# Optimization experiments

Measured on AMD Instinct MI355X. Metric: run time of the kernel, lower is better.

The kernel has to match this reference:

```python
import jax, jax.numpy as jnp
import numpy as np

N, F, DE = 768, 64, 32
H0, H1, H2, OUT = 64, 64, 128, 1  # hidden_dim=[64,64,128], output_dim=1


def _mlp(x, Wa, ba, Wb, bb):
    # two Dense layers with relu, as in the repo's MLP
    h = jax.nn.relu(x @ Wa + ba)
    return jax.nn.relu(h @ Wb + bb)


def _edge_conv_e(A, x, e, Wa, ba, Wb, bb):
    # EdgeConvE: per-edge message MLP([x_i, x_j - x_i, e_ij]) aggregated
    # over neighbors j weighted by the (binary) adjacency.
    n = x.shape[0]
    xi = jnp.broadcast_to(x[:, None, :], (n, n, x.shape[1]))  # [N,N,F]
    xj = jnp.broadcast_to(x[None, :, :], (n, n, x.shape[1]))  # [N,N,F]
    feat = jnp.concatenate([xi, xj - xi, e], axis=-1)         # [N,N,2F+De]
    m = _mlp(feat, Wa, ba, Wb, bb)                            # [N,N,H]
    return jnp.einsum('ij,ijh->ih', A, m)                     # scatter-sum over j


def setup_inputs() -> dict:
    key = jax.random.key(0)
    ks = jax.random.split(key, 16)
    adj = (jax.random.uniform(ks[0], (N, N)) < 0.05).astype(jnp.float32)
    x = jax.random.normal(ks[1], (N, F), dtype=jnp.float32)
    e = jax.random.normal(ks[2], (N, N, DE), dtype=jnp.float32)
    s = 0.05
    d_in1 = 2 * F + DE          # 160
    d_in2 = 2 * H0 + DE         # 160
    return {
        'ajacency': adj,
        'node_features': x,
        'edge_attributes': e,
        'W1a': jax.random.normal(ks[3], (d_in1, H0)) * s, 'b1a': jnp.zeros((H0,)),
        'W1b': jax.random.normal(ks[4], (H0, H0)) * s,    'b1b': jnp.zeros((H0,)),
        'W2a': jax.random.normal(ks[5], (d_in2, H1)) * s, 'b2a': jnp.zeros((H1,)),
        'W2b': jax.random.normal(ks[6], (H1, H0)) * s,    'b2b': jnp.zeros((H0,)),
        'W3': jax.random.normal(ks[7], (H0, H2)) * s,     'b3': jnp.zeros((H2,)),
        'W4': jax.random.normal(ks[8], (H2, OUT)) * s,    'b4': jnp.zeros((OUT,)),
    }


def reference(ajacency, node_features, edge_attributes,
              W1a, b1a, W1b, b1b, W2a, b2a, W2b, b2b, W3, b3, W4, b4):
    x = _edge_conv_e(ajacency, node_features, edge_attributes, W1a, b1a, W1b, b1b)
    x = _edge_conv_e(ajacency, x, edge_attributes, W2a, b2a, W2b, b2b)
    x = jax.nn.relu(x @ W3 + b3)
    return jax.nn.sigmoid(x @ W4 + b4)  # [N, OUT]
```

## Files before the change

### kernel.cpp

```cpp
#include <hip/hip_runtime.h>
#include <math.h>


#define NN 768
#define FF 64
#define DE 32
#define HH 64
#define EPB 32
#define CGRID 1024
#define ECAP (NN * 128)
#define SH1S 72

using bf16x8 = __attribute__((ext_vector_type(8))) short;
using f32x4  = __attribute__((ext_vector_type(4))) float;

__device__ __forceinline__ short f2b(float f) {
  unsigned u = __float_as_uint(f);
  return (short)((u + 0x7fffu + ((u >> 16) & 1u)) >> 16);
}

__global__ __launch_bounds__(256) void scan_uv_kernel(
    const float* __restrict__ A, const float* __restrict__ x,
    const float* __restrict__ W, const float* __restrict__ bias,
    const float* __restrict__ Wb1, const float* __restrict__ Wb2,
    int* __restrict__ gcnt, int* __restrict__ edges,
    float* __restrict__ U, float* __restrict__ V,
    float* __restrict__ x1, float* __restrict__ x2,
    short* __restrict__ Wbp1, short* __restrict__ Wbp2)
{
  const int i = blockIdx.x;
  const int tid = threadIdx.x;
  __shared__ int s_cnt, s_base;
  __shared__ int s_j[NN];
  __shared__ float sx[64];
  __shared__ float su[4][64], sv[4][64];

  if (tid == 0) s_cnt = 0;
  __syncthreads();
  if (tid < 64) sx[tid] = x[i * 64 + tid];
  for (int j = tid; j < NN; j += 256) {
    if (A[i * NN + j] != 0.0f) {
      int p = atomicAdd(&s_cnt, 1);
      s_j[p] = j;
    }
  }
  if (tid < 64) { x1[i * 64 + tid] = 0.0f; x2[i * 64 + tid] = 0.0f; }

  if (i < 2) {
    const float* src = (i == 0) ? Wb1 : Wb2;
    short* dst = (i == 0) ? Wbp1 : Wbp2;
    for (int L = tid; L < 4096; L += 256) {
      const int j = L & 7, n = (L >> 3) & 15, quad = (L >> 7) & 3;
      const int kb = (L >> 9) & 1, ct = L >> 10;
      dst[L] = f2b(src[(kb * 32 + quad * 8 + j) * 64 + ct * 16 + n]);
    }
  }
  __syncthreads();

  {
    const int c = tid & 63, qr = tid >> 6;
    float u = 0.0f, v = 0.0f;
#pragma unroll
    for (int t = 0; t < 16; ++t) {
      const int d = qr * 16 + t;
      const float xv = sx[d];
      const float wxi = W[d * 64 + c];
      const float wxj = W[(64 + d) * 64 + c];
      u = fmaf(xv, wxi - wxj, u);
      v = fmaf(xv, wxj, v);
    }
    su[qr][c] = u; sv[qr][c] = v;
  }
  if (tid == 0) s_base = atomicAdd(gcnt, s_cnt);
  __syncthreads();

  if (tid < 64) {
    U[i * 64 + tid] = su[0][tid] + su[1][tid] + su[2][tid] + su[3][tid] + bias[tid];
    V[i * 64 + tid] = sv[0][tid] + sv[1][tid] + sv[2][tid] + sv[3][tid];
  }
  const int c = s_cnt, b = s_base;
  for (int t = tid; t < c; t += 256) edges[b + t] = (i << 10) | s_j[t];
}

__global__ __launch_bounds__(256, 4) void uv_kernel(
    const float* __restrict__ x, const float* __restrict__ W,
    const float* __restrict__ bias, float* __restrict__ U, float* __restrict__ V)
{
  const int tid = threadIdx.x;
  const int rr = tid >> 6, c = tid & 63;
  const int r = blockIdx.x * 4 + rr;
  __shared__ float sx[4][64];
  sx[rr][c] = x[r * 64 + c];
  __syncthreads();
  float u = bias[c], v = 0.0f;
#pragma unroll
  for (int d = 0; d < 64; ++d) {
    float xv = sx[rr][d];
    float wxi = W[d * 64 + c];
    float wxj = W[(64 + d) * 64 + c];
    u = fmaf(xv, wxi - wxj, u);
    v = fmaf(xv, wxj, v);
  }
  U[r * 64 + c] = u;
  V[r * 64 + c] = v;
}

__device__ __forceinline__ void phaseB_mfma(
    const short* __restrict__ sh1b, const int* __restrict__ si,
    const short* __restrict__ Wbp, const float* __restrict__ bb,
    float* __restrict__ xout, int lane, int wv, int nedge)
{
  const int q = lane >> 4, n = lane & 15;
  const int rt = wv >> 1;
  const int ctbase = (wv & 1) * 2;

  bf16x8 bf00 = *(const bf16x8*)(Wbp + ((((ctbase + 0) * 2 + 0) * 4 + q) * 16 + n) * 8);
  bf16x8 bf01 = *(const bf16x8*)(Wbp + ((((ctbase + 0) * 2 + 1) * 4 + q) * 16 + n) * 8);
  bf16x8 bf10 = *(const bf16x8*)(Wbp + ((((ctbase + 1) * 2 + 0) * 4 + q) * 16 + n) * 8);
  bf16x8 bf11 = *(const bf16x8*)(Wbp + ((((ctbase + 1) * 2 + 1) * 4 + q) * 16 + n) * 8);
  const float bias0 = bb[(ctbase + 0) * 16 + n];
  const float bias1 = bb[(ctbase + 1) * 16 + n];

  const short* sa = sh1b + (rt * 16 + n) * SH1S + q * 8;
  bf16x8 a0 = *(const bf16x8*)(sa);
  bf16x8 a1 = *(const bf16x8*)(sa + 32);

  f32x4 acc0 = {0.f, 0.f, 0.f, 0.f}, acc1 = {0.f, 0.f, 0.f, 0.f};
  acc0 = __builtin_amdgcn_mfma_f32_16x16x32_bf16(a0, bf00, acc0, 0, 0, 0);
  acc0 = __builtin_amdgcn_mfma_f32_16x16x32_bf16(a1, bf01, acc0, 0, 0, 0);
  acc1 = __builtin_amdgcn_mfma_f32_16x16x32_bf16(a0, bf10, acc1, 0, 0, 0);
  acc1 = __builtin_amdgcn_mfma_f32_16x16x32_bf16(a1, bf11, acc1, 0, 0, 0);

#pragma unroll
  for (int c2 = 0; c2 < 2; ++c2) {
    const f32x4 d = c2 ? acc1 : acc0;
    const float bias = c2 ? bias1 : bias0;
    const int ch = (ctbase + c2) * 16 + n;
    float sum = 0.0f;
    int cur = -1;
#pragma unroll
    for (int reg = 0; reg < 4; ++reg) {
      const int t = rt * 16 + q * 4 + reg;
      if (t < nedge) {
        const int it = si[t];
        const float v = fmaxf(d[reg] + bias, 0.0f);
        if (it != cur) {
          if (cur >= 0) atomicAdd(&xout[(cur << 6) + ch], sum);
          sum = 0.0f;
          cur = it;
        }
        sum += v;
      }
    }
    if (cur >= 0) atomicAdd(&xout[(cur << 6) + ch], sum);
  }
}

__global__ void conv1_kernel(
    const int* __restrict__ gcnt, const int* __restrict__ edges,
    const float* __restrict__ U, const float* __restrict__ V,
    const float* __restrict__ e, const float* __restrict__ We1,
    const float* __restrict__ We2, const short* __restrict__ Wbp,
    const float* __restrict__ bb, float* __restrict__ xout,
    float* __restrict__ ew2)
{
  const int tid = threadIdx.x, lane = tid & 63, wv = tid >> 6;
  const int M = gcnt[0];
  const int base = blockIdx.x * EPB;
  if (base >= M) return;
  const int nedge = min(EPB, M - base);

  __shared__ __align__(16) short sh1b[EPB * SH1S];
  __shared__ int si[EPB];

  float w1e[DE], w2e[DE];
#pragma unroll
  for (int d = 0; d < DE; ++d) { w1e[d] = We1[d * HH + lane]; w2e[d] = We2[d * HH + lane]; }

  const int a0 = wv * 8;
#pragma unroll
  for (int t = 0; t < 8; ++t) {
    int m = base + a0 + t;
    const bool valid = m < M;
    m = valid ? m : M - 1;
    const int p = edges[m];
    const int i = p >> 10, j = p & 1023;
    float h = U[(i << 6) + lane] + V[(j << 6) + lane];
    float g = 0.0f;
    const float4* ep = (const float4*)(e + ((size_t)i * NN + j) * DE);
#pragma unroll
    for (int u = 0; u < 8; ++u) {
      float4 f = ep[u];
      h = fmaf(f.x, w1e[4 * u + 0], h);
      h = fmaf(f.y, w1e[4 * u + 1], h);
      h = fmaf(f.z, w1e[4 * u + 2], h);
      h = fmaf(f.w, w1e[4 * u + 3], h);
      g = fmaf(f.x, w2e[4 * u + 0], g);
      g = fmaf(f.y, w2e[4 * u + 1], g);
      g = fmaf(f.z, w2e[4 * u + 2], g);
      g = fmaf(f.w, w2e[4 * u + 3], g);
    }
    sh1b[(a0 + t) * SH1S + lane] = f2b(fmaxf(h, 0.0f));
    if (valid) ew2[(size_t)m * HH + lane] = g;
    if (lane == 0) si[a0 + t] = i;
  }
  __syncthreads();

  phaseB_mfma(sh1b, si, Wbp, bb, xout, lane, wv, nedge);
}

__global__ void conv2_kernel(
    const int* __restrict__ gcnt, const int* __restrict__ edges,
    const float* __restrict__ U, const float* __restrict__ V,
    const float* __restrict__ ew2, const short* __restrict__ Wbp,
    const float* __restrict__ bb, float* __restrict__ xout)
{
  const int tid = threadIdx.x, lane = tid & 63, wv = tid >> 6;
  const int M = gcnt[0];
  const int base = blockIdx.x * EPB;
  if (base >= M) return;
  const int nedge = min(EPB, M - base);

  __shared__ __align__(16) short sh1b[EPB * SH1S];
  __shared__ int si[EPB];

  const int a0 = wv * 8;
#pragma unroll
  for (int t = 0; t < 8; ++t) {
    int m = base + a0 + t;
    m = m < M ? m : M - 1;
    const int p = edges[m];
    const int i = p >> 10, j = p & 1023;
    const float h = U[(i << 6) + lane] + V[(j << 6) + lane]
                  + ew2[(size_t)m * HH + lane];
    sh1b[(a0 + t) * SH1S + lane] = f2b(fmaxf(h, 0.0f));
    if (lane == 0) si[a0 + t] = i;
  }
  __syncthreads();

  phaseB_mfma(sh1b, si, Wbp, bb, xout, lane, wv, nedge);
}

__global__ __launch_bounds__(128) void final_kernel(
    const float* __restrict__ x2, const float* __restrict__ W3,
    const float* __restrict__ b3, const float* __restrict__ W4,
    const float* __restrict__ b4, float* __restrict__ out)
{
  const int i = blockIdx.x;
  const int t = threadIdx.x;
  const int lane = t & 63;
  const int wv = t >> 6;
  __shared__ float sx[64];
  __shared__ float s_red[2];
  if (t < 64) sx[t] = x2[i * 64 + t];
  __syncthreads();
  float p = b3[t];
#pragma unroll
  for (int c = 0; c < 64; ++c) p = fmaf(sx[c], W3[c * 128 + t], p);
  p = fmaxf(p, 0.0f);
  float v = p * W4[t];
  v += __shfl_down(v, 32);
  v += __shfl_down(v, 16);
  v += __shfl_down(v, 8);
  v += __shfl_down(v, 4);
  v += __shfl_down(v, 2);
  v += __shfl_down(v, 1);
  if (lane == 0) s_red[wv] = v;
  __syncthreads();
  if (t == 0) {
    float z = s_red[0] + s_red[1] + b4[0];
    out[i] = 1.0f / (1.0f + expf(-z));
  }
}

extern "C" void kernel_launch(void* const* d_in, const int* in_sizes, int n_in,
                              void* d_out, int out_size, void* d_ws, size_t ws_size,
                              hipStream_t stream) {
  const float* A   = (const float*)d_in[0];
  const float* x   = (const float*)d_in[1];
  const float* e   = (const float*)d_in[2];
  const float* W1a = (const float*)d_in[3];
  const float* b1a = (const float*)d_in[4];
  const float* W1b = (const float*)d_in[5];
  const float* b1b = (const float*)d_in[6];
  const float* W2a = (const float*)d_in[7];
  const float* b2a = (const float*)d_in[8];
  const float* W2b = (const float*)d_in[9];
  const float* b2b = (const float*)d_in[10];
  const float* W3  = (const float*)d_in[11];
  const float* b3  = (const float*)d_in[12];
  const float* W4  = (const float*)d_in[13];
  const float* b4  = (const float*)d_in[14];
  float* out = (float*)d_out;

  int*   gcnt  = (int*)d_ws;
  float* x1    = (float*)d_ws + 16;
  float* x2    = x1 + NN * HH;
  float* U1    = x2 + NN * HH;
  float* V1    = U1 + NN * HH;
  float* U2    = V1 + NN * HH;
  float* V2    = U2 + NN * HH;
  int*   edges = (int*)(V2 + NN * HH);
  float* ew2   = (float*)(edges + ECAP);
  short* Wbp1  = (short*)(ew2 + (size_t)CGRID * EPB * HH);
  short* Wbp2  = Wbp1 + 4096;

  hipMemsetAsync(gcnt, 0, 16 * sizeof(int), stream);

  scan_uv_kernel<<<NN, 256, 0, stream>>>(A, x, W1a, b1a, W1b, W2b,
                                         gcnt, edges, U1, V1, x1, x2, Wbp1, Wbp2);
  conv1_kernel<<<CGRID, 256, 0, stream>>>(gcnt, edges, U1, V1, e,
                                          W1a + 128 * HH, W2a + 128 * HH,
                                          Wbp1, b1b, x1, ew2);
  uv_kernel<<<NN / 4, 256, 0, stream>>>(x1, W2a, b2a, U2, V2);
  conv2_kernel<<<CGRID, 256, 0, stream>>>(gcnt, edges, U2, V2, ew2,
                                          Wbp2, b2b, x2);
  final_kernel<<<NN, 128, 0, stream>>>(x2, W3, b3, W4, b4, out);
}
```

Measured before the change: 179.1 us.

## Fuse all five stages into one cooperative persistent kernel with grid syncs

```diff
diff --git a/kernel.cpp b/kernel.cpp
--- a/kernel.cpp
+++ b/kernel.cpp
@@ -1,5 +1,8 @@
 #include <hip/hip_runtime.h>
+#include <hip/hip_cooperative_groups.h>
 #include <math.h>
+
+namespace cg = cooperative_groups;
 
 
 #define NN 768
@@ -7,6 +10,7 @@
 #define DE 32
 #define HH 64
 #define EPB 32
+#define GRID 256
 #define CGRID 1024
 #define ECAP (NN * 128)
 #define SH1S 72
@@ -19,96 +23,10 @@
   return (short)((u + 0x7fffu + ((u >> 16) & 1u)) >> 16);
 }
 
-__global__ __launch_bounds__(256) void scan_uv_kernel(
-    const float* __restrict__ A, const float* __restrict__ x,
-    const float* __restrict__ W, const float* __restrict__ bias,
-    const float* __restrict__ Wb1, const float* __restrict__ Wb2,
-    int* __restrict__ gcnt, int* __restrict__ edges,
-    float* __restrict__ U, float* __restrict__ V,
-    float* __restrict__ x1, float* __restrict__ x2,
-    short* __restrict__ Wbp1, short* __restrict__ Wbp2)
-{
-  const int i = blockIdx.x;
-  const int tid = threadIdx.x;
-  __shared__ int s_cnt, s_base;
-  __shared__ int s_j[NN];
-  __shared__ float sx[64];
-  __shared__ float su[4][64], sv[4][64];
-
-  if (tid == 0) s_cnt = 0;
-  __syncthreads();
-  if (tid < 64) sx[tid] = x[i * 64 + tid];
-  for (int j = tid; j < NN; j += 256) {
-    if (A[i * NN + j] != 0.0f) {
-      int p = atomicAdd(&s_cnt, 1);
-      s_j[p] = j;
-    }
-  }
-  if (tid < 64) { x1[i * 64 + tid] = 0.0f; x2[i * 64 + tid] = 0.0f; }
-
-  if (i < 2) {
-    const float* src = (i == 0) ? Wb1 : Wb2;
-    short* dst = (i == 0) ? Wbp1 : Wbp2;
-    for (int L = tid; L < 4096; L += 256) {
-      const int j = L & 7, n = (L >> 3) & 15, quad = (L >> 7) & 3;
-      const int kb = (L >> 9) & 1, ct = L >> 10;
-      dst[L] = f2b(src[(kb * 32 + quad * 8 + j) * 64 + ct * 16 + n]);
-    }
-  }
-  __syncthreads();
-
-  {
-    const int c = tid & 63, qr = tid >> 6;
-    float u = 0.0f, v = 0.0f;
-#pragma unroll
-    for (int t = 0; t < 16; ++t) {
-      const int d = qr * 16 + t;
-      const float xv = sx[d];
-      const float wxi = W[d * 64 + c];
-      const float wxj = W[(64 + d) * 64 + c];
-      u = fmaf(xv, wxi - wxj, u);
-      v = fmaf(xv, wxj, v);
-    }
-    su[qr][c] = u; sv[qr][c] = v;
-  }
-  if (tid == 0) s_base = atomicAdd(gcnt, s_cnt);
-  __syncthreads();
-
-  if (tid < 64) {
-    U[i * 64 + tid] = su[0][tid] + su[1][tid] + su[2][tid] + su[3][tid] + bias[tid];
-    V[i * 64 + tid] = sv[0][tid] + sv[1][tid] + sv[2][tid] + sv[3][tid];
-  }
-  const int c = s_cnt, b = s_base;
-  for (int t = tid; t < c; t += 256) edges[b + t] = (i << 10) | s_j[t];
-}
-
-__global__ __launch_bounds__(256, 4) void uv_kernel(
-    const float* __restrict__ x, const float* __restrict__ W,
-    const float* __restrict__ bias, float* __restrict__ U, float* __restrict__ V)
-{
-  const int tid = threadIdx.x;
-  const int rr = tid >> 6, c = tid & 63;
-  const int r = blockIdx.x * 4 + rr;
-  __shared__ float sx[4][64];
-  sx[rr][c] = x[r * 64 + c];
-  __syncthreads();
-  float u = bias[c], v = 0.0f;
-#pragma unroll
-  for (int d = 0; d < 64; ++d) {
-    float xv = sx[rr][d];
-    float wxi = W[d * 64 + c];
-    float wxj = W[(64 + d) * 64 + c];
-    u = fmaf(xv, wxi - wxj, u);
-    v = fmaf(xv, wxj, v);
-  }
-  U[r * 64 + c] = u;
-  V[r * 64 + c] = v;
-}
-
 __device__ __forceinline__ void phaseB_mfma(
-    const short* __restrict__ sh1b, const int* __restrict__ si,
-    const short* __restrict__ Wbp, const float* __restrict__ bb,
-    float* __restrict__ xout, int lane, int wv, int nedge)
+    const short* sh1b, const int* si, const short* __restrict__ Wbp,
+    const float* __restrict__ bb, float* __restrict__ xout,
+    int lane, int wv, int nedge)
 {
   const int q = lane >> 4, n = lane & 15;
   const int rt = wv >> 1;
@@ -156,6 +74,282 @@
   }
 }
 
+__global__ __launch_bounds__(256, 2) void mega_kernel(
+    const float* __restrict__ A, const float* __restrict__ x,
+    const float* __restrict__ e,
+    const float* __restrict__ W1a, const float* __restrict__ b1a,
+    const float* __restrict__ W1b, const float* __restrict__ b1b,
+    const float* __restrict__ W2a, const float* __restrict__ b2a,
+    const float* __restrict__ W2b, const float* __restrict__ b2b,
+    const float* __restrict__ W3, const float* __restrict__ b3,
+    const float* __restrict__ W4, const float* __restrict__ b4,
+    float* __restrict__ out,
+    int* gcnt, int* edges, float* x1, float* x2,
+    float* U1, float* V1, float* U2, float* V2,
+    float* ew2, short* Wbp1, short* Wbp2)
+{
+  cg::grid_group grid = cg::this_grid();
+  const int tid = threadIdx.x, lane = tid & 63, wv = tid >> 6;
+  const int bid = blockIdx.x;
+
+  __shared__ int s_cnt, s_base;
+  __shared__ int s_j[NN];
+  __shared__ float sxr[64];
+  __shared__ float su[4][64], sv[4][64];
+  __shared__ __align__(16) short sh1b[EPB * SH1S];
+  __shared__ int si[EPB];
+  __shared__ float sred[4];
+
+  for (int i = bid; i < NN; i += GRID) {
+    __syncthreads();
+    if (tid == 0) s_cnt = 0;
+    __syncthreads();
+    if (tid < 64) sxr[tid] = x[i * 64 + tid];
+    for (int j = tid; j < NN; j += 256) {
+      if (A[i * NN + j] != 0.0f) {
+        int p = atomicAdd(&s_cnt, 1);
+        s_j[p] = j;
+      }
+    }
+    if (tid < 64) { x1[i * 64 + tid] = 0.0f; x2[i * 64 + tid] = 0.0f; }
+    __syncthreads();
+    {
+      const int c = tid & 63, qr = tid >> 6;
+      float u = 0.0f, v = 0.0f;
+#pragma unroll
+      for (int t = 0; t < 16; ++t) {
+        const int d = qr * 16 + t;
+        const float xv = sxr[d];
+        const float wxi = W1a[d * 64 + c];
+        const float wxj = W1a[(64 + d) * 64 + c];
+        u = fmaf(xv, wxi - wxj, u);
+        v = fmaf(xv, wxj, v);
+      }
+      su[qr][c] = u; sv[qr][c] = v;
+    }
+    if (tid == 0) s_base = atomicAdd(gcnt, s_cnt);
+    __syncthreads();
+    if (tid < 64) {
+      U1[i * 64 + tid] = su[0][tid] + su[1][tid] + su[2][tid] + su[3][tid] + b1a[tid];
+      V1[i * 64 + tid] = sv[0][tid] + sv[1][tid] + sv[2][tid] + sv[3][tid];
+    }
+    const int c = s_cnt, b = s_base;
+    for (int t = tid; t < c; t += 256) edges[b + t] = (i << 10) | s_j[t];
+  }
+  if (bid < 2) {
+    const float* src = (bid == 0) ? W1b : W2b;
+    short* dst = (bid == 0) ? Wbp1 : Wbp2;
+    for (int L = tid; L < 4096; L += 256) {
+      const int j = L & 7, n = (L >> 3) & 15, quad = (L >> 7) & 3;
+      const int kb = (L >> 9) & 1, ct = L >> 10;
+      dst[L] = f2b(src[(kb * 32 + quad * 8 + j) * 64 + ct * 16 + n]);
+    }
+  }
+  __threadfence();
+  grid.sync();
+  const int M = gcnt[0];
+
+  {
+    float w1e[DE], w2e[DE];
+#pragma unroll
+    for (int d = 0; d < DE; ++d) {
+      w1e[d] = W1a[(128 + d) * HH + lane];
+      w2e[d] = W2a[(128 + d) * HH + lane];
+    }
+    const int a0 = wv * 8;
+    for (int base = bid * EPB; base < M; base += GRID * EPB) {
+      const int nedge = min(EPB, M - base);
+#pragma unroll
+      for (int t = 0; t < 8; ++t) {
+        int m = base + a0 + t;
+        const bool valid = m < M;
+        m = valid ? m : M - 1;
+        const int p = edges[m];
+        const int i = p >> 10, j = p & 1023;
+        float h = U1[(i << 6) + lane] + V1[(j << 6) + lane];
+        float g = 0.0f;
+        const float4* ep = (const float4*)(e + ((size_t)i * NN + j) * DE);
+#pragma unroll
+        for (int u = 0; u < 8; ++u) {
+          float4 f = ep[u];
+          h = fmaf(f.x, w1e[4 * u + 0], h);
+          h = fmaf(f.y, w1e[4 * u + 1], h);
+          h = fmaf(f.z, w1e[4 * u + 2], h);
+          h = fmaf(f.w, w1e[4 * u + 3], h);
+          g = fmaf(f.x, w2e[4 * u + 0], g);
+          g = fmaf(f.y, w2e[4 * u + 1], g);
+          g = fmaf(f.z, w2e[4 * u + 2], g);
+          g = fmaf(f.w, w2e[4 * u + 3], g);
+        }
+        sh1b[(a0 + t) * SH1S + lane] = f2b(fmaxf(h, 0.0f));
+        if (valid) ew2[(size_t)m * HH + lane] = g;
+        if (lane == 0) si[a0 + t] = i;
+      }
+      __syncthreads();
+      phaseB_mfma(sh1b, si, Wbp1, b1b, x1, lane, wv, nedge);
+      __syncthreads();
+    }
+  }
+  __threadfence();
+  grid.sync();
+
+  for (int r4 = bid; r4 < NN / 4; r4 += GRID) {
+    const int rr = tid >> 6, c = tid & 63;
+    const int r = r4 * 4 + rr;
+    __syncthreads();
+    su[rr][c] = x1[r * 64 + c];
+    __syncthreads();
+    float u = b2a[c], v = 0.0f;
+#pragma unroll
+    for (int d = 0; d < 64; ++d) {
+      float xv = su[rr][d];
+      float wxi = W2a[d * 64 + c];
+      float wxj = W2a[(64 + d) * 64 + c];
+      u = fmaf(xv, wxi - wxj, u);
+      v = fmaf(xv, wxj, v);
+    }
+    U2[r * 64 + c] = u;
+    V2[r * 64 + c] = v;
+  }
+  __threadfence();
+  grid.sync();
+
+  {
+    const int a0 = wv * 8;
+    for (int base = bid * EPB; base < M; base += GRID * EPB) {
+      const int nedge = min(EPB, M - base);
+#pragma unroll
+      for (int t = 0; t < 8; ++t) {
+        int m = base + a0 + t;
+        m = m < M ? m : M - 1;
+        const int p = edges[m];
+        const int i = p >> 10, j = p & 1023;
+        const float h = U2[(i << 6) + lane] + V2[(j << 6) + lane]
+                      + ew2[(size_t)m * HH + lane];
+        sh1b[(a0 + t) * SH1S + lane] = f2b(fmaxf(h, 0.0f));
+        if (lane == 0) si[a0 + t] = i;
+      }
+      __syncthreads();
+      phaseB_mfma(sh1b, si, Wbp2, b2b, x2, lane, wv, nedge);
+      __syncthreads();
+    }
+  }
+  __threadfence();
+  grid.sync();
+
+  for (int i0 = bid * 2; i0 < NN; i0 += GRID * 2) {
+    const int half = tid >> 7;
+    const int t128 = tid & 127;
+    const int i = i0 + half;
+    __syncthreads();
+    if (t128 < 64) su[half * 2][t128] = x2[i * 64 + t128];
+    __syncthreads();
+    float p = b3[t128];
+#pragma unroll
+    for (int c = 0; c < 64; ++c) p = fmaf(su[half * 2][c], W3[c * 128 + t128], p);
+    p = fmaxf(p, 0.0f);
+    float v = p * W4[t128];
+    v += __shfl_down(v, 32);
+    v += __shfl_down(v, 16);
+    v += __shfl_down(v, 8);
+    v += __shfl_down(v, 4);
+    v += __shfl_down(v, 2);
+    v += __shfl_down(v, 1);
+    if (lane == 0) sred[wv] = v;
+    __syncthreads();
+    if (t128 == 0) {
+      float z = sred[half * 2] + sred[half * 2 + 1] + b4[0];
+      out[i] = 1.0f / (1.0f + expf(-z));
+    }
+  }
+}
+
+__global__ __launch_bounds__(256) void scan_uv_kernel(
+    const float* __restrict__ A, const float* __restrict__ x,
+    const float* __restrict__ W, const float* __restrict__ bias,
+    const float* __restrict__ Wb1, const float* __restrict__ Wb2,
+    int* __restrict__ gcnt, int* __restrict__ edges,
+    float* __restrict__ U, float* __restrict__ V,
+    float* __restrict__ x1, float* __restrict__ x2,
+    short* __restrict__ Wbp1, short* __restrict__ Wbp2)
+{
+  const int i = blockIdx.x;
+  const int tid = threadIdx.x;
+  __shared__ int s_cnt, s_base;
+  __shared__ int s_j[NN];
+  __shared__ float sx[64];
+  __shared__ float su[4][64], sv[4][64];
+
+  if (tid == 0) s_cnt = 0;
+  __syncthreads();
+  if (tid < 64) sx[tid] = x[i * 64 + tid];
+  for (int j = tid; j < NN; j += 256) {
+    if (A[i * NN + j] != 0.0f) {
+      int p = atomicAdd(&s_cnt, 1);
+      s_j[p] = j;
+    }
+  }
+  if (tid < 64) { x1[i * 64 + tid] = 0.0f; x2[i * 64 + tid] = 0.0f; }
+
+  if (i < 2) {
+    const float* src = (i == 0) ? Wb1 : Wb2;
+    short* dst = (i == 0) ? Wbp1 : Wbp2;
+    for (int L = tid; L < 4096; L += 256) {
+      const int j = L & 7, n = (L >> 3) & 15, quad = (L >> 7) & 3;
+      const int kb = (L >> 9) & 1, ct = L >> 10;
+      dst[L] = f2b(src[(kb * 32 + quad * 8 + j) * 64 + ct * 16 + n]);
+    }
+  }
+  __syncthreads();
+
+  {
+    const int c = tid & 63, qr = tid >> 6;
+    float u = 0.0f, v = 0.0f;
+#pragma unroll
+    for (int t = 0; t < 16; ++t) {
+      const int d = qr * 16 + t;
+      const float xv = sx[d];
+      const float wxi = W[d * 64 + c];
+      const float wxj = W[(64 + d) * 64 + c];
+      u = fmaf(xv, wxi - wxj, u);
+      v = fmaf(xv, wxj, v);
+    }
+    su[qr][c] = u; sv[qr][c] = v;
+  }
+  if (tid == 0) s_base = atomicAdd(gcnt, s_cnt);
+  __syncthreads();
+
+  if (tid < 64) {
+    U[i * 64 + tid] = su[0][tid] + su[1][tid] + su[2][tid] + su[3][tid] + bias[tid];
+    V[i * 64 + tid] = sv[0][tid] + sv[1][tid] + sv[2][tid] + sv[3][tid];
+  }
+  const int c = s_cnt, b = s_base;
+  for (int t = tid; t < c; t += 256) edges[b + t] = (i << 10) | s_j[t];
+}
+
+__global__ __launch_bounds__(256, 4) void uv_kernel(
+    const float* __restrict__ x, const float* __restrict__ W,
+    const float* __restrict__ bias, float* __restrict__ U, float* __restrict__ V)
+{
+  const int tid = threadIdx.x;
+  const int rr = tid >> 6, c = tid & 63;
+  const int r = blockIdx.x * 4 + rr;
+  __shared__ float sx[4][64];
+  sx[rr][c] = x[r * 64 + c];
+  __syncthreads();
+  float u = bias[c], v = 0.0f;
+#pragma unroll
+  for (int d = 0; d < 64; ++d) {
+    float xv = sx[rr][d];
+    float wxi = W[d * 64 + c];
+    float wxj = W[(64 + d) * 64 + c];
+    u = fmaf(xv, wxi - wxj, u);
+    v = fmaf(xv, wxj, v);
+  }
+  U[r * 64 + c] = u;
+  V[r * 64 + c] = v;
+}
+
 __global__ void conv1_kernel(
     const int* __restrict__ gcnt, const int* __restrict__ edges,
     const float* __restrict__ U, const float* __restrict__ V,
@@ -205,7 +399,6 @@
     if (lane == 0) si[a0 + t] = i;
   }
   __syncthreads();
-
   phaseB_mfma(sh1b, si, Wbp, bb, xout, lane, wv, nedge);
 }
 
@@ -237,7 +430,6 @@
     if (lane == 0) si[a0 + t] = i;
   }
   __syncthreads();
-
   phaseB_mfma(sh1b, si, Wbp, bb, xout, lane, wv, nedge);
 }
 
@@ -302,18 +494,32 @@
   float* V2    = U2 + NN * HH;
   int*   edges = (int*)(V2 + NN * HH);
   float* ew2   = (float*)(edges + ECAP);
-  short* Wbp1  = (short*)(ew2 + (size_t)CGRID * EPB * HH);
+  short* Wbp1  = (short*)(ew2 + (size_t)ECAP * HH);
   short* Wbp2  = Wbp1 + 4096;
 
   hipMemsetAsync(gcnt, 0, 16 * sizeof(int), stream);
 
-  scan_uv_kernel<<<NN, 256, 0, stream>>>(A, x, W1a, b1a, W1b, W2b,
-                                         gcnt, edges, U1, V1, x1, x2, Wbp1, Wbp2);
-  conv1_kernel<<<CGRID, 256, 0, stream>>>(gcnt, edges, U1, V1, e,
-                                          W1a + 128 * HH, W2a + 128 * HH,
-                                          Wbp1, b1b, x1, ew2);
-  uv_kernel<<<NN / 4, 256, 0, stream>>>(x1, W2a, b2a, U2, V2);
-  conv2_kernel<<<CGRID, 256, 0, stream>>>(gcnt, edges, U2, V2, ew2,
-                                          Wbp2, b2b, x2);
-  final_kernel<<<NN, 128, 0, stream>>>(x2, W3, b3, W4, b4, out);
-}
+  void* args[] = {
+    (void*)&A, (void*)&x, (void*)&e,
+    (void*)&W1a, (void*)&b1a, (void*)&W1b, (void*)&b1b,
+    (void*)&W2a, (void*)&b2a, (void*)&W2b, (void*)&b2b,
+    (void*)&W3, (void*)&b3, (void*)&W4, (void*)&b4,
+    (void*)&out,
+    (void*)&gcnt, (void*)&edges, (void*)&x1, (void*)&x2,
+    (void*)&U1, (void*)&V1, (void*)&U2, (void*)&V2,
+    (void*)&ew2, (void*)&Wbp1, (void*)&Wbp2,
+  };
+  hipError_t err = hipLaunchCooperativeKernel((void*)mega_kernel, dim3(GRID),
+                                              dim3(256), args, 0, stream);
+  if (err != hipSuccess) {
+    scan_uv_kernel<<<NN, 256, 0, stream>>>(A, x, W1a, b1a, W1b, W2b,
+                                           gcnt, edges, U1, V1, x1, x2, Wbp1, Wbp2);
+    conv1_kernel<<<CGRID, 256, 0, stream>>>(gcnt, edges, U1, V1, e,
+                                            W1a + 128 * HH, W2a + 128 * HH,
+                                            Wbp1, b1b, x1, ew2);
+    uv_kernel<<<NN / 4, 256, 0, stream>>>(x1, W2a, b2a, U2, V2);
+    conv2_kernel<<<CGRID, 256, 0, stream>>>(gcnt, edges, U2, V2, ew2,
+                                            Wbp2, b2b, x2);
+    final_kernel<<<NN, 128, 0, stream>>>(x2, W3, b3, W4, b4, out);
+  }
+}
```

Result: slower. 424.9 us (+137.3%).

## Replace global edge list with per-node CSR slots and per-node conv blocks

Applied to the files above, without the earlier changes.

```diff
diff --git a/kernel.cpp b/kernel.cpp
--- a/kernel.cpp
+++ b/kernel.cpp
@@ -6,9 +6,9 @@
 #define FF 64
 #define DE 32
 #define HH 64
-#define EPB 32
-#define CGRID 1024
-#define ECAP (NN * 128)
+#define EPB 16
+#define MAXB 8
+#define CAP 128
 #define SH1S 72
 
 using bf16x8 = __attribute__((ext_vector_type(8))) short;
@@ -23,14 +23,14 @@
     const float* __restrict__ A, const float* __restrict__ x,
     const float* __restrict__ W, const float* __restrict__ bias,
     const float* __restrict__ Wb1, const float* __restrict__ Wb2,
-    int* __restrict__ gcnt, int* __restrict__ edges,
+    int* __restrict__ cnt, int* __restrict__ jl,
     float* __restrict__ U, float* __restrict__ V,
     float* __restrict__ x1, float* __restrict__ x2,
     short* __restrict__ Wbp1, short* __restrict__ Wbp2)
 {
   const int i = blockIdx.x;
   const int tid = threadIdx.x;
-  __shared__ int s_cnt, s_base;
+  __shared__ int s_cnt;
   __shared__ int s_j[NN];
   __shared__ float sx[64];
   __shared__ float su[4][64], sv[4][64];
@@ -38,11 +38,12 @@
   if (tid == 0) s_cnt = 0;
   __syncthreads();
   if (tid < 64) sx[tid] = x[i * 64 + tid];
-  for (int j = tid; j < NN; j += 256) {
-    if (A[i * NN + j] != 0.0f) {
-      int p = atomicAdd(&s_cnt, 1);
-      s_j[p] = j;
-    }
+  if (tid < NN / 4) {
+    float4 a = ((const float4*)(A + i * NN))[tid];
+    if (a.x != 0.0f) { int p = atomicAdd(&s_cnt, 1); s_j[p] = tid * 4 + 0; }
+    if (a.y != 0.0f) { int p = atomicAdd(&s_cnt, 1); s_j[p] = tid * 4 + 1; }
+    if (a.z != 0.0f) { int p = atomicAdd(&s_cnt, 1); s_j[p] = tid * 4 + 2; }
+    if (a.w != 0.0f) { int p = atomicAdd(&s_cnt, 1); s_j[p] = tid * 4 + 3; }
   }
   if (tid < 64) { x1[i * 64 + tid] = 0.0f; x2[i * 64 + tid] = 0.0f; }
 
@@ -71,15 +72,15 @@
     }
     su[qr][c] = u; sv[qr][c] = v;
   }
-  if (tid == 0) s_base = atomicAdd(gcnt, s_cnt);
   __syncthreads();
 
   if (tid < 64) {
     U[i * 64 + tid] = su[0][tid] + su[1][tid] + su[2][tid] + su[3][tid] + bias[tid];
     V[i * 64 + tid] = sv[0][tid] + sv[1][tid] + sv[2][tid] + sv[3][tid];
   }
-  const int c = s_cnt, b = s_base;
-  for (int t = tid; t < c; t += 256) edges[b + t] = (i << 10) | s_j[t];
+  const int c = min(s_cnt, CAP);
+  if (tid == 0) cnt[i] = c;
+  for (int t = tid; t < c; t += 256) jl[(i << 7) + t] = s_j[t];
 }
 
 __global__ __launch_bounds__(256, 4) void uv_kernel(
@@ -105,89 +106,65 @@
   V[r * 64 + c] = v;
 }
 
-__device__ __forceinline__ void phaseB_mfma(
-    const short* __restrict__ sh1b, const int* __restrict__ si,
-    const short* __restrict__ Wbp, const float* __restrict__ bb,
-    float* __restrict__ xout, int lane, int wv, int nedge)
+__device__ __forceinline__ void phaseB16(
+    const short* sh1b, const short* __restrict__ Wbp,
+    const float* __restrict__ bb, float* __restrict__ xout,
+    int i, int lane, int wv, int nedge)
 {
   const int q = lane >> 4, n = lane & 15;
-  const int rt = wv >> 1;
-  const int ctbase = (wv & 1) * 2;
-
-  bf16x8 bf00 = *(const bf16x8*)(Wbp + ((((ctbase + 0) * 2 + 0) * 4 + q) * 16 + n) * 8);
-  bf16x8 bf01 = *(const bf16x8*)(Wbp + ((((ctbase + 0) * 2 + 1) * 4 + q) * 16 + n) * 8);
-  bf16x8 bf10 = *(const bf16x8*)(Wbp + ((((ctbase + 1) * 2 + 0) * 4 + q) * 16 + n) * 8);
-  bf16x8 bf11 = *(const bf16x8*)(Wbp + ((((ctbase + 1) * 2 + 1) * 4 + q) * 16 + n) * 8);
-  const float bias0 = bb[(ctbase + 0) * 16 + n];
-  const float bias1 = bb[(ctbase + 1) * 16 + n];
-
-  const short* sa = sh1b + (rt * 16 + n) * SH1S + q * 8;
+  bf16x8 b0 = *(const bf16x8*)(Wbp + (((wv * 2 + 0) * 4 + q) * 16 + n) * 8);
+  bf16x8 b1 = *(const bf16x8*)(Wbp + (((wv * 2 + 1) * 4 + q) * 16 + n) * 8);
+  const float bias = bb[wv * 16 + n];
+  const short* sa = sh1b + n * SH1S + q * 8;
   bf16x8 a0 = *(const bf16x8*)(sa);
   bf16x8 a1 = *(const bf16x8*)(sa + 32);
 
-  f32x4 acc0 = {0.f, 0.f, 0.f, 0.f}, acc1 = {0.f, 0.f, 0.f, 0.f};
-  acc0 = __builtin_amdgcn_mfma_f32_16x16x32_bf16(a0, bf00, acc0, 0, 0, 0);
-  acc0 = __builtin_amdgcn_mfma_f32_16x16x32_bf16(a1, bf01, acc0, 0, 0, 0);
-  acc1 = __builtin_amdgcn_mfma_f32_16x16x32_bf16(a0, bf10, acc1, 0, 0, 0);
-  acc1 = __builtin_amdgcn_mfma_f32_16x16x32_bf16(a1, bf11, acc1, 0, 0, 0);
-
-#pragma unroll
-  for (int c2 = 0; c2 < 2; ++c2) {
-    const f32x4 d = c2 ? acc1 : acc0;
-    const float bias = c2 ? bias1 : bias0;
-    const int ch = (ctbase + c2) * 16 + n;
-    float sum = 0.0f;
-    int cur = -1;
-#pragma unroll
-    for (int reg = 0; reg < 4; ++reg) {
-      const int t = rt * 16 + q * 4 + reg;
-      if (t < nedge) {
-        const int it = si[t];
-        const float v = fmaxf(d[reg] + bias, 0.0f);
-        if (it != cur) {
-          if (cur >= 0) atomicAdd(&xout[(cur << 6) + ch], sum);
-          sum = 0.0f;
-          cur = it;
-        }
-        sum += v;
-      }
-    }
-    if (cur >= 0) atomicAdd(&xout[(cur << 6) + ch], sum);
-  }
-}
-
-__global__ void conv1_kernel(
-    const int* __restrict__ gcnt, const int* __restrict__ edges,
+  f32x4 acc = {0.f, 0.f, 0.f, 0.f};
+  acc = __builtin_amdgcn_mfma_f32_16x16x32_bf16(a0, b0, acc, 0, 0, 0);
+  acc = __builtin_amdgcn_mfma_f32_16x16x32_bf16(a1, b1, acc, 0, 0, 0);
+
+  float s = 0.0f;
+#pragma unroll
+  for (int reg = 0; reg < 4; ++reg) {
+    const int row = q * 4 + reg;
+    const float v = fmaxf(acc[reg] + bias, 0.0f);
+    s += (row < nedge) ? v : 0.0f;
+  }
+  s += __shfl_down(s, 32);
+  s += __shfl_down(s, 16);
+  if (lane < 16) atomicAdd(&xout[(i << 6) + wv * 16 + lane], s);
+}
+
+__global__ __launch_bounds__(256) void conv1_kernel(
+    const int* __restrict__ cnt, const int* __restrict__ jl,
     const float* __restrict__ U, const float* __restrict__ V,
     const float* __restrict__ e, const float* __restrict__ We1,
     const float* __restrict__ We2, const short* __restrict__ Wbp,
     const float* __restrict__ bb, float* __restrict__ xout,
     float* __restrict__ ew2)
 {
+  const int i = blockIdx.x >> 3;
+  const int t0 = (blockIdx.x & (MAXB - 1)) * EPB;
+  const int c = cnt[i];
+  if (t0 >= c) return;
+  const int nedge = min(EPB, c - t0);
+
   const int tid = threadIdx.x, lane = tid & 63, wv = tid >> 6;
-  const int M = gcnt[0];
-  const int base = blockIdx.x * EPB;
-  if (base >= M) return;
-  const int nedge = min(EPB, M - base);
-
   __shared__ __align__(16) short sh1b[EPB * SH1S];
-  __shared__ int si[EPB];
 
   float w1e[DE], w2e[DE];
 #pragma unroll
   for (int d = 0; d < DE; ++d) { w1e[d] = We1[d * HH + lane]; w2e[d] = We2[d * HH + lane]; }
 
-  const int a0 = wv * 8;
-#pragma unroll
-  for (int t = 0; t < 8; ++t) {
-    int m = base + a0 + t;
-    const bool valid = m < M;
-    m = valid ? m : M - 1;
-    const int p = edges[m];
-    const int i = p >> 10, j = p & 1023;
-    float h = U[(i << 6) + lane] + V[(j << 6) + lane];
+  const float u_i = U[(i << 6) + lane];
+#pragma unroll
+  for (int t = 0; t < 4; ++t) {
+    const int slot = wv * 4 + t;
+    const int idx = t0 + (slot < nedge ? slot : nedge - 1);
+    const int j = jl[(i << 7) + idx];
+    float h = u_i + V[(j << 6) + lane];
     float g = 0.0f;
-    const float4* ep = (const float4*)(e + ((size_t)i * NN + j) * DE);
+    const float4* ep = (const float4*)(e + ((size_t)(i * NN + j)) * DE);
 #pragma unroll
     for (int u = 0; u < 8; ++u) {
       float4 f = ep[u];
@@ -200,45 +177,40 @@
       g = fmaf(f.z, w2e[4 * u + 2], g);
       g = fmaf(f.w, w2e[4 * u + 3], g);
     }
-    sh1b[(a0 + t) * SH1S + lane] = f2b(fmaxf(h, 0.0f));
-    if (valid) ew2[(size_t)m * HH + lane] = g;
-    if (lane == 0) si[a0 + t] = i;
-  }
-  __syncthreads();
-
-  phaseB_mfma(sh1b, si, Wbp, bb, xout, lane, wv, nedge);
-}
-
-__global__ void conv2_kernel(
-    const int* __restrict__ gcnt, const int* __restrict__ edges,
+    sh1b[slot * SH1S + lane] = f2b(fmaxf(h, 0.0f));
+    if (slot < nedge) ew2[((size_t)(i << 7) + t0 + slot) * HH + lane] = g;
+  }
+  __syncthreads();
+  phaseB16(sh1b, Wbp, bb, xout, i, lane, wv, nedge);
+}
+
+__global__ __launch_bounds__(256) void conv2_kernel(
+    const int* __restrict__ cnt, const int* __restrict__ jl,
     const float* __restrict__ U, const float* __restrict__ V,
     const float* __restrict__ ew2, const short* __restrict__ Wbp,
     const float* __restrict__ bb, float* __restrict__ xout)
 {
+  const int i = blockIdx.x >> 3;
+  const int t0 = (blockIdx.x & (MAXB - 1)) * EPB;
+  const int c = cnt[i];
+  if (t0 >= c) return;
+  const int nedge = min(EPB, c - t0);
+
   const int tid = threadIdx.x, lane = tid & 63, wv = tid >> 6;
-  const int M = gcnt[0];
-  const int base = blockIdx.x * EPB;
-  if (base >= M) return;
-  const int nedge = min(EPB, M - base);
-
   __shared__ __align__(16) short sh1b[EPB * SH1S];
-  __shared__ int si[EPB];
-
-  const int a0 = wv * 8;
-#pragma unroll
-  for (int t = 0; t < 8; ++t) {
-    int m = base + a0 + t;
-    m = m < M ? m : M - 1;
-    const int p = edges[m];
-    const int i = p >> 10, j = p & 1023;
-    const float h = U[(i << 6) + lane] + V[(j << 6) + lane]
-                  + ew2[(size_t)m * HH + lane];
-    sh1b[(a0 + t) * SH1S + lane] = f2b(fmaxf(h, 0.0f));
-    if (lane == 0) si[a0 + t] = i;
-  }
-  __syncthreads();
-
-  phaseB_mfma(sh1b, si, Wbp, bb, xout, lane, wv, nedge);
+
+  const float u_i = U[(i << 6) + lane];
+#pragma unroll
+  for (int t = 0; t < 4; ++t) {
+    const int slot = wv * 4 + t;
+    const int idx = t0 + (slot < nedge ? slot : nedge - 1);
+    const int j = jl[(i << 7) + idx];
+    const float h = u_i + V[(j << 6) + lane]
+                  + ew2[((size_t)(i << 7) + idx) * HH + lane];
+    sh1b[slot * SH1S + lane] = f2b(fmaxf(h, 0.0f));
+  }
+  __syncthreads();
+  phaseB16(sh1b, Wbp, bb, xout, i, lane, wv, nedge);
 }
 
 __global__ __launch_bounds__(128) void final_kernel(
@@ -293,27 +265,25 @@
   const float* b4  = (const float*)d_in[14];
   float* out = (float*)d_out;
 
-  int*   gcnt  = (int*)d_ws;
-  float* x1    = (float*)d_ws + 16;
-  float* x2    = x1 + NN * HH;
-  float* U1    = x2 + NN * HH;
-  float* V1    = U1 + NN * HH;
-  float* U2    = V1 + NN * HH;
-  float* V2    = U2 + NN * HH;
-  int*   edges = (int*)(V2 + NN * HH);
-  float* ew2   = (float*)(edges + ECAP);
-  short* Wbp1  = (short*)(ew2 + (size_t)CGRID * EPB * HH);
-  short* Wbp2  = Wbp1 + 4096;
-
-  hipMemsetAsync(gcnt, 0, 16 * sizeof(int), stream);
+  int*   cnt  = (int*)d_ws;
+  int*   jl   = cnt + NN;
+  float* x1   = (float*)(jl + NN * CAP);
+  float* x2   = x1 + NN * HH;
+  float* U1   = x2 + NN * HH;
+  float* V1   = U1 + NN * HH;
+  float* U2   = V1 + NN * HH;
+  float* V2   = U2 + NN * HH;
+  float* ew2  = V2 + NN * HH;
+  short* Wbp1 = (short*)(ew2 + (size_t)NN * CAP * HH);
+  short* Wbp2 = Wbp1 + 4096;
 
   scan_uv_kernel<<<NN, 256, 0, stream>>>(A, x, W1a, b1a, W1b, W2b,
-                                         gcnt, edges, U1, V1, x1, x2, Wbp1, Wbp2);
-  conv1_kernel<<<CGRID, 256, 0, stream>>>(gcnt, edges, U1, V1, e,
-                                          W1a + 128 * HH, W2a + 128 * HH,
-                                          Wbp1, b1b, x1, ew2);
+                                         cnt, jl, U1, V1, x1, x2, Wbp1, Wbp2);
+  conv1_kernel<<<NN * MAXB, 256, 0, stream>>>(cnt, jl, U1, V1, e,
+                                              W1a + 128 * HH, W2a + 128 * HH,
+                                              Wbp1, b1b, x1, ew2);
   uv_kernel<<<NN / 4, 256, 0, stream>>>(x1, W2a, b2a, U2, V2);
-  conv2_kernel<<<CGRID, 256, 0, stream>>>(gcnt, edges, U2, V2, ew2,
-                                          Wbp2, b2b, x2);
+  conv2_kernel<<<NN * MAXB, 256, 0, stream>>>(cnt, jl, U2, V2, ew2,
+                                              Wbp2, b2b, x2);
   final_kernel<<<NN, 128, 0, stream>>>(x2, W3, b3, W4, b4, out);
 }
```

Result: slower. 188.9 us (+5.5%).
